# Performance work log

Hardware: AMD Instinct MI355X
Metric: run time of the kernel (lower is better)

Reference implementation:

```python
import jax, jax.numpy as jnp
import numpy as np

T, D_IN, H, KV, HD = 1024, 2048, 32, 8, 64
GROUP = H // KV  # 4
EPS = 1e-6


def _rmsnorm(x, w):
    inv_rms = jax.lax.rsqrt(jnp.mean(x * x, axis=-1, keepdims=True) + EPS)
    return x * inv_rms * w


def _rope(x, cos, sin):
    # x: [heads, T, HD]; cos/sin: [T, HD]
    hd = x.shape[-1]
    x1, x2 = x[..., : hd // 2], x[..., hd // 2 :]
    rotated = jnp.concatenate([-x2, x1], axis=-1)
    return x * cos[None, :, :] + rotated * sin[None, :, :]


def setup_inputs() -> dict:
    key = jax.random.key(0)
    ks = jax.random.split(key, 6)
    x = jax.random.normal(ks[0], (T, D_IN), dtype=jnp.float32)
    # RoPE tables (cos/sin over [T, HD])
    inv_freq = 1.0 / (10000.0 ** (np.arange(0, HD, 2, dtype=np.float64) / HD))
    ang = np.arange(T, dtype=np.float64)[:, None] * inv_freq[None, :]
    emb = np.concatenate([ang, ang], axis=-1)
    cos = jnp.asarray(np.cos(emb), dtype=jnp.float32)
    sin = jnp.asarray(np.sin(emb), dtype=jnp.float32)
    # causal mask: True above diagonal -> masked to -inf
    mask = jnp.triu(jnp.ones((T, T), dtype=jnp.bool_), k=1)
    # kaiming_normal fan_in (relu): std = sqrt(2/fan_in)
    Wq = jax.random.normal(ks[1], (H * HD, D_IN), jnp.float32) * (2.0 / D_IN) ** 0.5
    Wk = jax.random.normal(ks[2], (KV * HD, D_IN), jnp.float32) * (2.0 / D_IN) ** 0.5
    Wv = jax.random.normal(ks[3], (KV * HD, D_IN), jnp.float32) * (2.0 / D_IN) ** 0.5
    Wo = jax.random.normal(ks[4], (D_IN, H * HD), jnp.float32) * (2.0 / (H * HD)) ** 0.5
    q_norm_w = jnp.ones((HD,), jnp.float32)
    k_norm_w = jnp.ones((HD,), jnp.float32)
    one = jnp.ones((1,), jnp.float32)
    return {
        "x": x, "scale_x": one, "mask": mask,
        "cos": cos, "scale_cos": one, "sin": sin, "scale_sin": one,
        "Wq": Wq, "Wk": Wk, "Wv": Wv, "Wo": Wo,
        "q_norm_w": q_norm_w, "k_norm_w": k_norm_w,
    }


def reference(x, scale_x, mask, cos, scale_cos, sin, scale_sin,
              Wq, Wk, Wv, Wo, q_norm_w, k_norm_w):
    num_tokens = x.shape[0]
    # QKV projections
    q = (x @ Wq.T).reshape(num_tokens, H, HD).transpose(1, 0, 2)   # [H, T, HD]
    k = (x @ Wk.T).reshape(num_tokens, KV, HD).transpose(1, 0, 2)  # [KV, T, HD]
    v = (x @ Wv.T).reshape(num_tokens, KV, HD).transpose(1, 0, 2)  # [KV, T, HD]
    # qk_norm
    q = _rmsnorm(q, q_norm_w)
    k = _rmsnorm(k, k_norm_w)
    # RoPE
    q = _rope(q, cos, sin)
    k = _rope(k, cos, sin)
    # expand KV groups to all heads (repeat_interleave along head axis)
    k = jnp.repeat(k, GROUP, axis=0)  # [H, T, HD]
    v = jnp.repeat(v, GROUP, axis=0)  # [H, T, HD]
    # attention scores
    qk = jnp.einsum("htd,hsd->hts", q, k) / (HD ** 0.5)
    qk = jnp.where(mask[None, :, :], -jnp.inf, qk)
    attn = jax.nn.softmax(qk, axis=-1)
    out = jnp.einsum("hts,hsd->htd", attn, v)          # [H, T, HD]
    out = out.transpose(1, 0, 2).reshape(num_tokens, H * HD)
    return out @ Wo.T  # [T, D_IN]
```

## Files before the change

kernel.cpp:

```cpp
#include <hip/hip_runtime.h>

typedef __bf16 bf16x8 __attribute__((ext_vector_type(8)));
typedef float f32x4 __attribute__((ext_vector_type(4)));

#define T_TOK 1024
#define DIN   2048
#define NH    32
#define NKV   8
#define HD    64

__device__ __forceinline__ unsigned short f2bf(float f) {
  unsigned int u = __float_as_uint(f);
  unsigned int r = (u + 0x7fffu + ((u >> 16) & 1u)) >> 16;
  return (unsigned short)r;
}

__device__ __forceinline__ void glds16(const void* g, void* lds) {
  __builtin_amdgcn_global_load_lds(
      (const __attribute__((address_space(1))) void*)g,
      (__attribute__((address_space(3))) void*)lds, 16, 0, 0);
}

__global__ __launch_bounds__(256) void k_cvt_all(
    const float* __restrict__ x,  const float* __restrict__ wq,
    const float* __restrict__ wk, const float* __restrict__ wv,
    const float* __restrict__ wo, unsigned short* __restrict__ xb,
    unsigned short* __restrict__ wqkv, unsigned short* __restrict__ wob) {
  const long NX = 1l << 21, NWQ = 1l << 22, NWK = 1l << 20, NWV = 1l << 20;
  long i4 = ((long)blockIdx.x * blockDim.x + threadIdx.x) * 4;
  const float* src;
  unsigned short* dst;
  long off;
  if (i4 < NX)                       { src = x;  dst = xb;   off = i4; }
  else if (i4 < NX + NWQ)            { src = wq; dst = wqkv; off = i4 - NX; }
  else if (i4 < NX + NWQ + NWK)      { src = wk; dst = wqkv + NWQ; off = i4 - NX - NWQ; }
  else if (i4 < NX + NWQ + NWK + NWV){ src = wv; dst = wqkv + NWQ + NWK; off = i4 - NX - NWQ - NWK; }
  else                               { src = wo; dst = wob;  off = i4 - NX - NWQ - NWK - NWV; }
  float4 v = *reinterpret_cast<const float4*>(src + off);
  ushort4 o;
  o.x = f2bf(v.x); o.y = f2bf(v.y); o.z = f2bf(v.z); o.w = f2bf(v.w);
  *reinterpret_cast<ushort4*>(dst + off) = o;
}

__global__ __launch_bounds__(256) void k_gemm2(
    const unsigned short* __restrict__ A, const unsigned short* __restrict__ B,
    float* __restrict__ C, int N, int K) {
  __shared__ unsigned short As[2][64 * 64];
  __shared__ unsigned short Bs[2][128 * 64];
  const int lane = threadIdx.x & 63;
  const int wave = threadIdx.x >> 6;
  const int wm = wave >> 1, wn = wave & 1;
  const int lr = lane & 15, lk = lane >> 4;
  const int brow = blockIdx.y * 64;
  const int bcol = blockIdx.x * 128;

  const int srow = lane >> 3;
  const int scol = ((lane & 7) ^ srow) * 8;
  const unsigned short* Ag = A + (long)(brow + srow) * K + scol;
  const unsigned short* Bg = B + (long)(bcol + srow) * K + scol;

  f32x4 acc[2][4];
#pragma unroll
  for (int i = 0; i < 2; i++)
#pragma unroll
    for (int j = 0; j < 4; j++) acc[i][j] = (f32x4){0.f, 0.f, 0.f, 0.f};

  const int swz = (lr & 7) << 4;
  const int nt = K / 64;
  int cur = 0;

#pragma unroll
  for (int i = 0; i < 2; i++) {
    int strip = i * 4 + wave;
    glds16(Ag + (long)strip * 8 * K, (char*)As[0] + strip * 1024);
  }
#pragma unroll
  for (int i = 0; i < 4; i++) {
    int strip = i * 4 + wave;
    glds16(Bg + (long)strip * 8 * K, (char*)Bs[0] + strip * 1024);
  }
  __syncthreads();

  for (int t = 0; t < nt; t++) {
    if (t + 1 < nt) {
      const int kk = (t + 1) * 64;
#pragma unroll
      for (int i = 0; i < 2; i++) {
        int strip = i * 4 + wave;
        glds16(Ag + (long)strip * 8 * K + kk, (char*)As[cur ^ 1] + strip * 1024);
      }
#pragma unroll
      for (int i = 0; i < 4; i++) {
        int strip = i * 4 + wave;
        glds16(Bg + (long)strip * 8 * K + kk, (char*)Bs[cur ^ 1] + strip * 1024);
      }
    }
#pragma unroll
    for (int s = 0; s < 2; s++) {
      bf16x8 a[2], b[4];
#pragma unroll
      for (int i = 0; i < 2; i++) {
        int row = wm * 32 + i * 16 + lr;
        a[i] = *reinterpret_cast<const bf16x8*>(
            (const char*)As[cur] + row * 128 + ((s * 64 + lk * 16) ^ swz));
      }
#pragma unroll
      for (int j = 0; j < 4; j++) {
        int row = wn * 64 + j * 16 + lr;
        b[j] = *reinterpret_cast<const bf16x8*>(
            (const char*)Bs[cur] + row * 128 + ((s * 64 + lk * 16) ^ swz));
      }
#pragma unroll
      for (int i = 0; i < 2; i++)
#pragma unroll
        for (int j = 0; j < 4; j++)
          acc[i][j] = __builtin_amdgcn_mfma_f32_16x16x32_bf16(a[i], b[j], acc[i][j], 0, 0, 0);
    }
    __syncthreads();
    cur ^= 1;
  }

#pragma unroll
  for (int i = 0; i < 2; i++)
#pragma unroll
    for (int j = 0; j < 4; j++)
#pragma unroll
      for (int p = 0; p < 4; p++)
        C[(long)(brow + wm * 32 + i * 16 + lk * 4 + p) * N + (bcol + wn * 64 + j * 16 + lr)] =
            acc[i][j][p];
}

__global__ void k_norm_rope(const float* __restrict__ qkv_lin,
                            unsigned short* __restrict__ qb, unsigned short* __restrict__ kb,
                            const float* __restrict__ cosT, const float* __restrict__ sinT,
                            const float* __restrict__ qw, const float* __restrict__ kw) {
  int gw = (blockIdx.x * blockDim.x + threadIdx.x) >> 6;
  int lane = threadIdx.x & 63;
  int t = gw / (NH + NKV);
  int hh = gw % (NH + NKV);
  if (t >= T_TOK) return;
  const float* base;
  unsigned short* ob;
  const float* w;
  if (hh < NH) {
    base = qkv_lin + (long)t * 3072 + hh * HD;
    ob   = qb + (long)t * (NH * HD) + hh * HD;
    w = qw;
  } else {
    int kh = hh - NH;
    base = qkv_lin + (long)t * 3072 + 2048 + kh * HD;
    ob   = kb + (long)t * (NKV * HD) + kh * HD;
    w = kw;
  }
  float v = base[lane];
  float ss = v * v;
#pragma unroll
  for (int off = 1; off < 64; off <<= 1) ss += __shfl_xor(ss, off);
  float xn = v * rsqrtf(ss * (1.0f / HD) + 1e-6f) * w[lane];
  float other = __shfl_xor(xn, 32);
  float c = cosT[t * HD + lane], s = sinT[t * HD + lane];
  ob[lane] = f2bf(xn * c + (lane < 32 ? -other : other) * s);
}

__global__ __launch_bounds__(256) void k_vt(const float* __restrict__ qkv_lin,
                                            unsigned short* __restrict__ out) {
  __shared__ float t[32][33];
  int tx = threadIdx.x & 31, ty = threadIdx.x >> 5;
  int r0 = blockIdx.y * 32;
  int c0 = blockIdx.x * 32;
#pragma unroll
  for (int r = 0; r < 4; r++)
    t[ty + r * 8][tx] = qkv_lin[(long)(r0 + ty + r * 8) * 3072 + 2560 + c0 + tx];
  __syncthreads();
#pragma unroll
  for (int r = 0; r < 4; r++)
    out[(long)(c0 + ty + r * 8) * 1024 + r0 + tx] = f2bf(t[tx][ty + r * 8]);
}

#define LOADK(K0, K1, tile) do {                                               \
    const unsigned short* kp_ = kb + (long)((tile) * 64 + lr) * 512 + kvh * 64 + lk * 8; \
    _Pragma("unroll") for (int f_ = 0; f_ < 4; f_++) {                         \
      K0[f_] = *reinterpret_cast<const bf16x8*>(kp_ + (long)f_ * 16 * 512);    \
      K1[f_] = *reinterpret_cast<const bf16x8*>(kp_ + (long)f_ * 16 * 512 + 32); \
    }                                                                          \
  } while (0)

#define BODY(KC0, KC1, KN0, KN1, tile) do {                                    \
    const int s0_ = (tile) * 64;                                               \
    const unsigned short* vp_ = vtb + (long)(kvh * 64 + lr) * 1024 + s0_ + lk * 8; \
    bf16x8 vfr[8];                                                             \
    _Pragma("unroll") for (int fd = 0; fd < 4; fd++) {                         \
      vfr[fd]     = *reinterpret_cast<const bf16x8*>(vp_ + (long)fd * 16 * 1024);      \
      vfr[4 + fd] = *reinterpret_cast<const bf16x8*>(vp_ + (long)fd * 16 * 1024 + 32); \
    }                                                                          \
    f32x4 sacc[4];                                                             \
    __builtin_amdgcn_s_setprio(1);                                             \
    _Pragma("unroll") for (int f = 0; f < 4; f++) {                            \
      sacc[f] = __builtin_amdgcn_mfma_f32_16x16x32_bf16(KC0[f], qa0, z4, 0, 0, 0);      \
      sacc[f] = __builtin_amdgcn_mfma_f32_16x16x32_bf16(KC1[f], qa1, sacc[f], 0, 0, 0); \
    }                                                                          \
    __builtin_amdgcn_s_setprio(0);                                             \
    if ((tile) + 1 < ntiles) LOADK(KN0, KN1, (tile) + 1);                      \
    const bool diag_ = ((tile) == qt);                                         \
    float sv[4][4];                                                            \
    float tmax_ = -3.0e38f;                                                    \
    _Pragma("unroll") for (int f = 0; f < 4; f++)                              \
      _Pragma("unroll") for (int p = 0; p < 4; p++) {                          \
        float s_ = sacc[f][p] * SC;                                            \
        if (diag_ && (f * 16 + lk * 4 + p) > qrel) s_ = -3.0e38f;              \
        sv[f][p] = s_;                                                         \
        tmax_ = fmaxf(tmax_, s_);                                              \
      }                                                                        \
    tmax_ = fmaxf(tmax_, __shfl_xor(tmax_, 16));                               \
    tmax_ = fmaxf(tmax_, __shfl_xor(tmax_, 32));                               \
    float mn_ = fmaxf(m2, tmax_);                                              \
    float r_ = exp2f(m2 - mn_);                                                \
    m2 = mn_;                                                                  \
    float rp_[4];                                                              \
    _Pragma("unroll") for (int p = 0; p < 4; p++)                              \
      rp_[p] = __shfl(r_, (lane & 48) | (lk * 4 + p));                         \
    float ps_ = 0.f;                                                           \
    _Pragma("unroll") for (int f = 0; f < 4; f++) {                            \
      float e0 = exp2f(sv[f][0] - mn_), e1 = exp2f(sv[f][1] - mn_);            \
      float e2 = exp2f(sv[f][2] - mn_), e3 = exp2f(sv[f][3] - mn_);            \
      ps_ += (e0 + e1) + (e2 + e3);                                            \
      uint2 pk_;                                                               \
      pk_.x = (unsigned)f2bf(e0) | ((unsigned)f2bf(e1) << 16);                 \
      pk_.y = (unsigned)f2bf(e2) | ((unsigned)f2bf(e3) << 16);                 \
      *reinterpret_cast<uint2*>(pbase + lr * 128 + ((f * 32 + lk * 8) ^ pswz)) = pk_; \
    }                                                                          \
    lp = lp * r_ + ps_;                                                        \
    _Pragma("unroll") for (int fd = 0; fd < 4; fd++)                           \
      _Pragma("unroll") for (int p = 0; p < 4; p++) o[fd][p] *= rp_[p];        \
    __builtin_amdgcn_s_setprio(1);                                             \
    _Pragma("unroll") for (int ks = 0; ks < 2; ks++) {                         \
      bf16x8 pa_ = *reinterpret_cast<const bf16x8*>(                           \
          pbase + lr * 128 + ((ks * 64 + lk * 16) ^ pswz));                    \
      _Pragma("unroll") for (int fd = 0; fd < 4; fd++)                         \
        o[fd] = __builtin_amdgcn_mfma_f32_16x16x32_bf16(pa_, vfr[ks * 4 + fd], o[fd], 0, 0, 0); \
    }                                                                          \
    __builtin_amdgcn_s_setprio(0);                                             \
  } while (0)

__global__ __launch_bounds__(256) void k_flash(
    const unsigned short* __restrict__ qb, const unsigned short* __restrict__ kb,
    const unsigned short* __restrict__ vtb, unsigned short* __restrict__ ao) {
  __shared__ unsigned short plds[4 * 16 * 64];
  const int h = blockIdx.y;
  const int qt = gridDim.x - 1 - blockIdx.x;
  const int kvh = h >> 2;
  const int lane = threadIdx.x & 63;
  const int wave = threadIdx.x >> 6;
  const int lr = lane & 15, lk = lane >> 4;
  const int qrow = qt * 64 + wave * 16;
  const int qrel = wave * 16 + lr;
  const int pswz = (lr & 7) << 4;
  char* pbase = (char*)plds + wave * 2048;
  const float SC = 0.125f * 1.44269504f;
  const f32x4 z4 = {0.f, 0.f, 0.f, 0.f};

  const unsigned short* qp = qb + (long)(qrow + lr) * (NH * HD) + h * HD + lk * 8;
  bf16x8 qa0 = *reinterpret_cast<const bf16x8*>(qp);
  bf16x8 qa1 = *reinterpret_cast<const bf16x8*>(qp + 32);

  f32x4 o[4];
#pragma unroll
  for (int f = 0; f < 4; f++) o[f] = z4;
  float m2 = -3.0e38f;
  float lp = 0.f;

  const int ntiles = qt + 1;
  bf16x8 kA0[4], kA1[4], kB0[4], kB1[4];
  LOADK(kA0, kA1, 0);
  for (int t = 0; t < ntiles; t += 2) {
    BODY(kA0, kA1, kB0, kB1, t);
    if (t + 1 >= ntiles) break;
    BODY(kB0, kB1, kA0, kA1, t + 1);
  }

  lp += __shfl_xor(lp, 16);
  lp += __shfl_xor(lp, 32);
  float lo[4];
#pragma unroll
  for (int p = 0; p < 4; p++) lo[p] = __shfl(lp, (lane & 48) | (lk * 4 + p));
#pragma unroll
  for (int fd = 0; fd < 4; fd++)
#pragma unroll
    for (int p = 0; p < 4; p++) {
      int qg = qrow + lk * 4 + p;
      int d = fd * 16 + lr;
      ao[(long)qg * (NH * HD) + h * HD + d] = f2bf(o[fd][p] / lo[p]);
    }
}

extern "C" void kernel_launch(void* const* d_in, const int* in_sizes, int n_in,
                              void* d_out, int out_size, void* d_ws, size_t ws_size,
                              hipStream_t stream) {
  const float* x    = (const float*)d_in[0];
  const float* cosT = (const float*)d_in[3];
  const float* sinT = (const float*)d_in[5];
  const float* Wq   = (const float*)d_in[7];
  const float* Wk   = (const float*)d_in[8];
  const float* Wv   = (const float*)d_in[9];
  const float* Wo   = (const float*)d_in[10];
  const float* qw   = (const float*)d_in[11];
  const float* kw   = (const float*)d_in[12];
  float* out = (float*)d_out;

  char* ws = (char*)d_ws;
  unsigned short* xb    = (unsigned short*)(ws);
  unsigned short* Wqkv  = (unsigned short*)(ws + (4u << 20));
  unsigned short* Wob   = (unsigned short*)(ws + (16u << 20));
  float* qkv_lin = (float*)(ws + (24u << 20));
  unsigned short* qbb = (unsigned short*)(ws + (36u << 20));
  unsigned short* kbb = (unsigned short*)(ws + (40u << 20));
  unsigned short* vtb = (unsigned short*)(ws + (41u << 20));
  unsigned short* ao  = (unsigned short*)(ws + (42u << 20));

  k_cvt_all<<<12288, 256, 0, stream>>>(x, Wq, Wk, Wv, Wo, xb, Wqkv, Wob);

  k_gemm2<<<dim3(24, 16), 256, 0, stream>>>(xb, Wqkv, qkv_lin, 3072, 2048);

  k_norm_rope<<<(T_TOK * (NH + NKV) * 64) / 256, 256, 0, stream>>>(
      qkv_lin, qbb, kbb, cosT, sinT, qw, kw);

  k_vt<<<dim3(16, 32), 256, 0, stream>>>(qkv_lin, vtb);

  k_flash<<<dim3(16, 32), 256, 0, stream>>>(qbb, kbb, vtb, ao);

  k_gemm2<<<dim3(16, 16), 256, 0, stream>>>(ao, Wob, out, 2048, 2048);
}
```

Baseline: 237.8 us.

## Split attention KV range across blocks and merge partials in combine kernel

The flash attention kernel now splits each query tile's key tiles across NSPLIT=4 blocks along grid z. Each block takes an interleaved subset of key tiles and writes unnormalized bf16 partial outputs plus per-row max and sum. A new combine kernel rescales and merges the partials into the attention output. The aim is more blocks and better load balance for the causal triangle on a large GPU. In exchange it adds a launch, about 16MB of partial traffic written and read back, and bf16 rounding of the unnormalized partials. It also sets a min-blocks-per-CU launch bound.

Result: slower. 284.0 us (+19.4%).

```diff
diff --git a/kernel.cpp b/kernel.cpp
--- a/kernel.cpp
+++ b/kernel.cpp
@@ -8,11 +8,16 @@
 #define NH    32
 #define NKV   8
 #define HD    64
+#define NSPLIT 4
 
 __device__ __forceinline__ unsigned short f2bf(float f) {
   unsigned int u = __float_as_uint(f);
   unsigned int r = (u + 0x7fffu + ((u >> 16) & 1u)) >> 16;
   return (unsigned short)r;
+}
+
+__device__ __forceinline__ float bf2f(unsigned short u) {
+  return __uint_as_float((unsigned int)u << 16);
 }
 
 __device__ __forceinline__ void glds16(const void* g, void* lds) {
@@ -200,7 +205,7 @@
       sacc[f] = __builtin_amdgcn_mfma_f32_16x16x32_bf16(KC1[f], qa1, sacc[f], 0, 0, 0); \
     }                                                                          \
     __builtin_amdgcn_s_setprio(0);                                             \
-    if ((tile) + 1 < ntiles) LOADK(KN0, KN1, (tile) + 1);                      \
+    if ((tile) + NSPLIT < ntiles) LOADK(KN0, KN1, (tile) + NSPLIT);            \
     const bool diag_ = ((tile) == qt);                                         \
     float sv[4][4];                                                            \
     float tmax_ = -3.0e38f;                                                    \
@@ -242,12 +247,15 @@
     __builtin_amdgcn_s_setprio(0);                                             \
   } while (0)
 
-__global__ __launch_bounds__(256) void k_flash(
+__global__ __launch_bounds__(256, 4) void k_flash(
     const unsigned short* __restrict__ qb, const unsigned short* __restrict__ kb,
-    const unsigned short* __restrict__ vtb, unsigned short* __restrict__ ao) {
+    const unsigned short* __restrict__ vtb, unsigned short* __restrict__ Opart,
+    float2* __restrict__ ml) {
+  const int qt = blockIdx.x;
+  const int h  = blockIdx.y;
+  const int sp = blockIdx.z;
+  if (sp > qt) return;
   __shared__ unsigned short plds[4 * 16 * 64];
-  const int h = blockIdx.y;
-  const int qt = gridDim.x - 1 - blockIdx.x;
   const int kvh = h >> 2;
   const int lane = threadIdx.x & 63;
   const int wave = threadIdx.x >> 6;
@@ -271,26 +279,55 @@
 
   const int ntiles = qt + 1;
   bf16x8 kA0[4], kA1[4], kB0[4], kB1[4];
-  LOADK(kA0, kA1, 0);
-  for (int t = 0; t < ntiles; t += 2) {
+  LOADK(kA0, kA1, sp);
+  for (int t = sp; t < ntiles; t += 2 * NSPLIT) {
     BODY(kA0, kA1, kB0, kB1, t);
-    if (t + 1 >= ntiles) break;
-    BODY(kB0, kB1, kA0, kA1, t + 1);
+    if (t + NSPLIT >= ntiles) break;
+    BODY(kB0, kB1, kA0, kA1, t + NSPLIT);
   }
 
   lp += __shfl_xor(lp, 16);
   lp += __shfl_xor(lp, 32);
-  float lo[4];
-#pragma unroll
-  for (int p = 0; p < 4; p++) lo[p] = __shfl(lp, (lane & 48) | (lk * 4 + p));
+  if (lk == 0) {
+    float2 mlv; mlv.x = m2; mlv.y = lp;
+    ml[((long)sp * NH + h) * T_TOK + qrow + lr] = mlv;
+  }
 #pragma unroll
   for (int fd = 0; fd < 4; fd++)
 #pragma unroll
     for (int p = 0; p < 4; p++) {
-      int qg = qrow + lk * 4 + p;
-      int d = fd * 16 + lr;
-      ao[(long)qg * (NH * HD) + h * HD + d] = f2bf(o[fd][p] / lo[p]);
+      long row = ((long)sp * NH + h) * T_TOK + qrow + lk * 4 + p;
+      Opart[row * HD + fd * 16 + lr] = f2bf(o[fd][p]);
     }
+}
+
+__global__ __launch_bounds__(256) void k_comb(
+    const unsigned short* __restrict__ Opart, const float2* __restrict__ ml,
+    unsigned short* __restrict__ ao) {
+  int w = (blockIdx.x * blockDim.x + threadIdx.x) >> 6;
+  int lane = threadIdx.x & 63;
+  int h = w >> 10, t = w & 1023;
+  int qt = t >> 6;
+  int nv = min(qt + 1, NSPLIT);
+  float mv[NSPLIT], lv[NSPLIT];
+  float M = -3.0e38f;
+#pragma unroll
+  for (int i = 0; i < NSPLIT; i++) {
+    if (i < nv) {
+      float2 x = ml[((long)i * NH + h) * T_TOK + t];
+      mv[i] = x.x; lv[i] = x.y;
+    } else { mv[i] = -3.0e38f; lv[i] = 0.f; }
+    M = fmaxf(M, mv[i]);
+  }
+  float L = 0.f, O = 0.f;
+#pragma unroll
+  for (int i = 0; i < NSPLIT; i++) {
+    float wgt = exp2f(mv[i] - M);
+    L += lv[i] * wgt;
+    float ov = (i < nv) ? bf2f(Opart[(((long)i * NH + h) * T_TOK + t) * HD + lane]) : 0.f;
+    O += ov * wgt;
+  }
+  ao[(long)t * (NH * HD) + h * HD + lane] = f2bf(O / L);
 }
 
 extern "C" void kernel_launch(void* const* d_in, const int* in_sizes, int n_in,
@@ -310,12 +347,14 @@
   char* ws = (char*)d_ws;
   unsigned short* xb    = (unsigned short*)(ws);
   unsigned short* Wqkv  = (unsigned short*)(ws + (4u << 20));
+  float* qkv_lin = (float*)(ws + (24u << 20));
   unsigned short* Wob   = (unsigned short*)(ws + (16u << 20));
-  float* qkv_lin = (float*)(ws + (24u << 20));
   unsigned short* qbb = (unsigned short*)(ws + (36u << 20));
   unsigned short* kbb = (unsigned short*)(ws + (40u << 20));
   unsigned short* vtb = (unsigned short*)(ws + (41u << 20));
   unsigned short* ao  = (unsigned short*)(ws + (42u << 20));
+  unsigned short* Opart = (unsigned short*)(ws);
+  float2* mlp           = (float2*)(ws + (24u << 20));
 
   k_cvt_all<<<12288, 256, 0, stream>>>(x, Wq, Wk, Wv, Wo, xb, Wqkv, Wob);
 
@@ -326,7 +365,9 @@
 
   k_vt<<<dim3(16, 32), 256, 0, stream>>>(qkv_lin, vtb);
 
-  k_flash<<<dim3(16, 32), 256, 0, stream>>>(qbb, kbb, vtb, ao);
+  k_flash<<<dim3(16, 32, NSPLIT), 256, 0, stream>>>(qbb, kbb, vtb, Opart, mlp);
+
+  k_comb<<<NH * T_TOK / 4, 256, 0, stream>>>(Opart, mlp, ao);
 
   k_gemm2<<<dim3(16, 16), 256, 0, stream>>>(ao, Wob, out, 2048, 2048);
 }
```

## Shrink GEMM N-tile to 64 and split flash attention into single-wave blocks

Applied to the files above, without the earlier changes.

The GEMM kernel is templated on the N tile width, and both projections now use 64-wide tiles, which doubles the grid size to fill more compute units. Flash attention moves from 4-wave blocks covering 64 query rows to 1-wave blocks covering 16 rows. This gives finer load balancing across the causal triangle and more resident blocks. The cost is less B-operand reuse per tile in the GEMMs and more redundant K/V loads across the smaller attention blocks.

Result: slower. 267.4 us (+12.4%).

```diff
diff --git a/kernel.cpp b/kernel.cpp
--- a/kernel.cpp
+++ b/kernel.cpp
@@ -42,28 +42,31 @@
   *reinterpret_cast<ushort4*>(dst + off) = o;
 }
 
+template<int BN>
 __global__ __launch_bounds__(256) void k_gemm2(
     const unsigned short* __restrict__ A, const unsigned short* __restrict__ B,
     float* __restrict__ C, int N, int K) {
+  constexpr int NJ = BN / 32;
+  constexpr int NBS = BN / 32;
   __shared__ unsigned short As[2][64 * 64];
-  __shared__ unsigned short Bs[2][128 * 64];
+  __shared__ unsigned short Bs[2][BN * 64];
   const int lane = threadIdx.x & 63;
   const int wave = threadIdx.x >> 6;
   const int wm = wave >> 1, wn = wave & 1;
   const int lr = lane & 15, lk = lane >> 4;
   const int brow = blockIdx.y * 64;
-  const int bcol = blockIdx.x * 128;
+  const int bcol = blockIdx.x * BN;
 
   const int srow = lane >> 3;
   const int scol = ((lane & 7) ^ srow) * 8;
   const unsigned short* Ag = A + (long)(brow + srow) * K + scol;
   const unsigned short* Bg = B + (long)(bcol + srow) * K + scol;
 
-  f32x4 acc[2][4];
+  f32x4 acc[2][NJ];
 #pragma unroll
   for (int i = 0; i < 2; i++)
 #pragma unroll
-    for (int j = 0; j < 4; j++) acc[i][j] = (f32x4){0.f, 0.f, 0.f, 0.f};
+    for (int j = 0; j < NJ; j++) acc[i][j] = (f32x4){0.f, 0.f, 0.f, 0.f};
 
   const int swz = (lr & 7) << 4;
   const int nt = K / 64;
@@ -75,7 +78,7 @@
     glds16(Ag + (long)strip * 8 * K, (char*)As[0] + strip * 1024);
   }
 #pragma unroll
-  for (int i = 0; i < 4; i++) {
+  for (int i = 0; i < NBS; i++) {
     int strip = i * 4 + wave;
     glds16(Bg + (long)strip * 8 * K, (char*)Bs[0] + strip * 1024);
   }
@@ -90,14 +93,14 @@
         glds16(Ag + (long)strip * 8 * K + kk, (char*)As[cur ^ 1] + strip * 1024);
       }
 #pragma unroll
-      for (int i = 0; i < 4; i++) {
+      for (int i = 0; i < NBS; i++) {
         int strip = i * 4 + wave;
         glds16(Bg + (long)strip * 8 * K + kk, (char*)Bs[cur ^ 1] + strip * 1024);
       }
     }
 #pragma unroll
     for (int s = 0; s < 2; s++) {
-      bf16x8 a[2], b[4];
+      bf16x8 a[2], b[NJ];
 #pragma unroll
       for (int i = 0; i < 2; i++) {
         int row = wm * 32 + i * 16 + lr;
@@ -105,15 +108,15 @@
             (const char*)As[cur] + row * 128 + ((s * 64 + lk * 16) ^ swz));
       }
 #pragma unroll
-      for (int j = 0; j < 4; j++) {
-        int row = wn * 64 + j * 16 + lr;
+      for (int j = 0; j < NJ; j++) {
+        int row = wn * (BN / 2) + j * 16 + lr;
         b[j] = *reinterpret_cast<const bf16x8*>(
             (const char*)Bs[cur] + row * 128 + ((s * 64 + lk * 16) ^ swz));
       }
 #pragma unroll
       for (int i = 0; i < 2; i++)
 #pragma unroll
-        for (int j = 0; j < 4; j++)
+        for (int j = 0; j < NJ; j++)
           acc[i][j] = __builtin_amdgcn_mfma_f32_16x16x32_bf16(a[i], b[j], acc[i][j], 0, 0, 0);
     }
     __syncthreads();
@@ -123,11 +126,11 @@
 #pragma unroll
   for (int i = 0; i < 2; i++)
 #pragma unroll
-    for (int j = 0; j < 4; j++)
+    for (int j = 0; j < NJ; j++)
 #pragma unroll
       for (int p = 0; p < 4; p++)
-        C[(long)(brow + wm * 32 + i * 16 + lk * 4 + p) * N + (bcol + wn * 64 + j * 16 + lr)] =
-            acc[i][j][p];
+        C[(long)(brow + wm * 32 + i * 16 + lk * 4 + p) * N +
+          (bcol + wn * (BN / 2) + j * 16 + lr)] = acc[i][j][p];
 }
 
 __global__ void k_norm_rope(const float* __restrict__ qkv_lin,
@@ -242,20 +245,20 @@
     __builtin_amdgcn_s_setprio(0);                                             \
   } while (0)
 
-__global__ __launch_bounds__(256) void k_flash(
+__global__ __launch_bounds__(64, 4) void k_flash(
     const unsigned short* __restrict__ qb, const unsigned short* __restrict__ kb,
     const unsigned short* __restrict__ vtb, unsigned short* __restrict__ ao) {
-  __shared__ unsigned short plds[4 * 16 * 64];
-  const int h = blockIdx.y;
-  const int qt = gridDim.x - 1 - blockIdx.x;
+  __shared__ unsigned short plds[16 * 64];
+  const int rb = 63 - blockIdx.x;
+  const int h  = blockIdx.y;
   const int kvh = h >> 2;
   const int lane = threadIdx.x & 63;
-  const int wave = threadIdx.x >> 6;
   const int lr = lane & 15, lk = lane >> 4;
-  const int qrow = qt * 64 + wave * 16;
-  const int qrel = wave * 16 + lr;
+  const int qrow = rb * 16;
+  const int qt = rb >> 2;
+  const int qrel = (rb & 3) * 16 + lr;
   const int pswz = (lr & 7) << 4;
-  char* pbase = (char*)plds + wave * 2048;
+  char* pbase = (char*)plds;
   const float SC = 0.125f * 1.44269504f;
   const f32x4 z4 = {0.f, 0.f, 0.f, 0.f};
 
@@ -319,14 +322,14 @@
 
   k_cvt_all<<<12288, 256, 0, stream>>>(x, Wq, Wk, Wv, Wo, xb, Wqkv, Wob);
 
-  k_gemm2<<<dim3(24, 16), 256, 0, stream>>>(xb, Wqkv, qkv_lin, 3072, 2048);
+  k_gemm2<64><<<dim3(48, 16), 256, 0, stream>>>(xb, Wqkv, qkv_lin, 3072, 2048);
 
   k_norm_rope<<<(T_TOK * (NH + NKV) * 64) / 256, 256, 0, stream>>>(
       qkv_lin, qbb, kbb, cosT, sinT, qw, kw);
 
   k_vt<<<dim3(16, 32), 256, 0, stream>>>(qkv_lin, vtb);
 
-  k_flash<<<dim3(16, 32), 256, 0, stream>>>(qbb, kbb, vtb, ao);
-
-  k_gemm2<<<dim3(16, 16), 256, 0, stream>>>(ao, Wob, out, 2048, 2048);
-}
+  k_flash<<<dim3(64, 32), 64, 0, stream>>>(qbb, kbb, vtb, ao);
+
+  k_gemm2<64><<<dim3(32, 16), 256, 0, stream>>>(ao, Wob, out, 2048, 2048);
+}
```
